# Kernel tuning notes

Hardware: AMD Instinct MI355X
Metric: run time of the kernel (lower is better)

Reference implementation:

```python
import jax, jax.numpy as jnp
import numpy as np

B, P, M, N, H, K, EH = 16, 50, 512, 1024, 64, 20, 200


def setup_inputs() -> dict:
    key = jax.random.key(0)
    ks = jax.random.split(key, 16)
    b = jax.random.normal(ks[0], (B, P, M, 1), jnp.float32)
    A = jax.random.normal(ks[1], (1, P, M, N), jnp.float32) / np.float32(np.sqrt(M))
    # random undirected multigraph on P nodes, stored with both directions
    s = jax.random.randint(ks[2], (B, EH), 0, P)
    off = jax.random.randint(ks[3], (B, EH), 1, P)
    d = (s + off) % P
    edge_index = jnp.stack([jnp.concatenate([s, d], 1), jnp.concatenate([d, s], 1)], 1).astype(jnp.int32)  # [B,2,2*EH]

    def lin(k, fi, fo, scale=None):
        scale = np.float32(1.0 / np.sqrt(fi)) if scale is None else np.float32(scale)
        return jax.random.normal(k, (fi, fo), jnp.float32) * scale, jnp.zeros((fo,), jnp.float32)

    W_e1, b_e1 = lin(ks[4], P * M, P * H)
    W_e2, b_e2 = lin(ks[5], P * H, 2 * P * H)
    W_e3, b_e3 = lin(ks[6], 2 * P * H, 4 * P * H)
    W_c1, b_c1 = lin(ks[7], 4 * H, 2 * H)
    W_c2, b_c2 = lin(ks[8], 2 * H, 2 * H)
    W_f1, b_f1 = lin(ks[9], 2 * H, H)
    W_f2, _ = lin(ks[10], H, K * 4, scale=1e-3)
    b_f2 = jnp.full((K * 4,), -2.0, jnp.float32)  # mimics fc2 init (tiny weights, negative bias)
    max_param = jnp.array([0.01, 0.1, 0.1, 0.1], jnp.float32).reshape(1, 1, 1, 4)  # [alpha,tau,rho,eta]_max
    y0 = jax.random.normal(ks[11], (B, P, N, 1), jnp.float32) * 0.01
    u0 = jax.random.normal(ks[12], (B, P, N, 1), jnp.float32) * 0.01
    d0 = jax.random.normal(ks[13], (B, P, N, 1), jnp.float32) * 0.01
    return dict(b=b, A=A, edge_index=edge_index, max_param=max_param,
                W_e1=W_e1, b_e1=b_e1, W_e2=W_e2, b_e2=b_e2, W_e3=W_e3, b_e3=b_e3,
                W_c1=W_c1, b_c1=b_c1, W_c2=W_c2, b_c2=b_c2,
                W_f1=W_f1, b_f1=b_f1, W_f2=W_f2, b_f2=b_f2,
                y0=y0, u0=u0, d0=d0)


def _lrelu(x):
    return jax.nn.leaky_relu(x, 0.01)


def _gcn(x, s, d, W, bias):
    # GCNConv: sym-normalized propagation with self loops. x: [P,F]
    h = x @ W
    deg = jnp.zeros((x.shape[0],), x.dtype).at[d].add(1.0) + 1.0  # +1 self loop
    dinv = jax.lax.rsqrt(deg)
    agg = jnp.zeros_like(h).at[d].add(h[s] * (dinv[s] * dinv[d])[:, None])
    agg = agg + h * (dinv * dinv)[:, None]  # self-loop term
    return agg + bias


def _delta(y, s, d):
    # nested neighbor loop: for each directed edge (s,d): delta[s]+=y[s]-y[d]; delta[d]-=same
    diff = y[s] - y[d]  # [E,N,1]
    return jnp.zeros_like(y).at[s].add(diff).at[d].add(-diff)


def reference(b, A, edge_index, max_param,
              W_e1, b_e1, W_e2, b_e2, W_e3, b_e3,
              W_c1, b_c1, W_c2, b_c2, W_f1, b_f1, W_f2, b_f2,
              y0, u0, d0):
    Bb = b.shape[0]
    n = A.shape[3]
    k_steps = W_f2.shape[1] // 4
    src, dst = edge_index[:, 0], edge_index[:, 1]

    # ---- GNN hypernetwork ----
    x = b.reshape(Bb, -1)
    x = _lrelu(x @ W_e1 + b_e1)
    x = _lrelu(x @ W_e2 + b_e2)
    x = (x @ W_e3 + b_e3).reshape(Bb, P, -1)  # [B,P,4H]
    x = _lrelu(jax.vmap(lambda xf, s, d: _gcn(xf, s, d, W_c1, b_c1))(x, src, dst))
    x = _lrelu(jax.vmap(lambda xf, s, d: _gcn(xf, s, d, W_c2, b_c2))(x, src, dst))
    x = x.mean(axis=1)  # global_mean_pool over nodes
    x = _lrelu(x @ W_f1 + b_f1)
    hyp = (x @ W_f2 + b_f2).reshape(Bb, k_steps, 1, 4)
    hyp = jax.nn.sigmoid(jnp.cumsum(hyp, axis=1)) * max_param  # [B,K,1,4]
    hyp_scan = jnp.transpose(hyp, (1, 3, 0, 2))[..., None, None]  # [K,4,B,1,1,1]

    # ---- precompute ----
    A0 = A[0]  # [P,M,N]
    AtA = jnp.einsum('pmn,pmk->pnk', A0, A0)  # [P,N,N]
    Atb = jnp.einsum('pmn,bpmo->bpno', A0, b)  # [B,P,N,1]
    sum_nb = jax.vmap(lambda s: jnp.zeros((P,), b.dtype).at[s].add(1.0))(src)[:, :, None, None]  # [B,P,1,1]

    # ---- unrolled D-ADMM / DLASSO ----
    def step(carry, hk):
        y_k, U_k, dlt = carry
        alpha, tau, rho, eta = hk[0], hk[1], hk[2], hk[3]
        AtAy = jnp.einsum('pnk,bpko->bpno', AtA, y_k)
        g = AtAy - Atb + jnp.sign(y_k) * tau + U_k * sum_nb + dlt * rho
        y_n = y_k - alpha * g
        dlt_n = jax.vmap(_delta)(y_n, src, dst)
        U_n = U_k + dlt_n * eta
        return (y_n, U_n, dlt_n), y_n

    _, Y = jax.lax.scan(step, (y0, u0, d0), hyp_scan)
    return Y  # [K,B,P,N,1]
```

## Files before the change

kernel.cpp:

```cpp
#include <hip/hip_runtime.h>

namespace {
constexpr int NB = 16;
constexpr int NP = 50;
constexpr int NM = 512;
constexpr int NN = 1024;
constexpr int NK = 20;
constexpr long ASZ = (long)NP * NM * NN;
constexpr long YSZ = (long)NB * NP * NN;
}

typedef __attribute__((ext_vector_type(8))) short bf16x8;
typedef __attribute__((ext_vector_type(4))) float f32x4;

__device__ __forceinline__ float lrelu(float x){ return x > 0.f ? x : 0.01f*x; }
__device__ __forceinline__ unsigned short f2bf(float f){
  unsigned u = __builtin_bit_cast(unsigned, f);
  u += 0x7fffu + ((u >> 16) & 1u);
  return (unsigned short)(u >> 16);
}

__global__ __launch_bounds__(256) void k_prep(const float* __restrict__ A,
                      unsigned short* __restrict__ abf, unsigned short* __restrict__ abfT){
  const int p = blockIdx.x, mt = blockIdx.y, nt = blockIdx.z;
  const int tid = threadIdx.x;
  __shared__ unsigned short tile[64][72];
  const int m0 = mt*64, n0 = nt*64;
  {
    int r = tid>>2, cs = (tid&3)*16;
    const float* src = A + ((long)p*NM + m0 + r)*NN + n0 + cs;
    unsigned short tmp[16];
    #pragma unroll
    for (int q=0;q<16;q+=4){
      float4 v = *(const float4*)(src+q);
      tmp[q+0]=f2bf(v.x); tmp[q+1]=f2bf(v.y); tmp[q+2]=f2bf(v.z); tmp[q+3]=f2bf(v.w);
    }
    #pragma unroll
    for (int q=0;q<16;q++) tile[r][cs+q] = tmp[q];
    unsigned short* dst = abf + ((long)p*NM + m0 + r)*NN + n0 + cs;
    #pragma unroll
    for (int q=0;q<16;q+=8) *(uint4*)(dst+q) = *(const uint4*)&tmp[q];
  }
  __syncthreads();
  {
    int r = tid>>2, cs = (tid&3)*16;
    unsigned short* dst = abfT + ((long)p*NN + n0 + r)*NM + m0 + cs;
    unsigned short tmp[16];
    #pragma unroll
    for (int q=0;q<16;q++) tmp[q] = tile[cs+q][r];
    #pragma unroll
    for (int q=0;q<16;q+=8) *(uint4*)(dst+q) = *(const uint4*)&tmp[q];
  }
}

__global__ void k_init(const float* __restrict__ y0, const float* __restrict__ u0,
                       const float* __restrict__ d0, float* __restrict__ y,
                       float* __restrict__ u, float* __restrict__ dl,
                       unsigned short* __restrict__ ybf, int n){
  int e = (blockIdx.x*blockDim.x + threadIdx.x)*4;
  if (e >= n) return;
  float4 a = *(const float4*)(y0+e);
  *(float4*)(y+e) = a;
  ushort4 o; o.x=f2bf(a.x); o.y=f2bf(a.y); o.z=f2bf(a.z); o.w=f2bf(a.w);
  *(ushort4*)(ybf+e) = o;
  *(float4*)(u+e)  = *(const float4*)(u0+e);
  *(float4*)(dl+e) = *(const float4*)(d0+e);
}

__global__ __launch_bounds__(256) void k_enc2(const float* __restrict__ X, const float* __restrict__ W,
                           float* __restrict__ part, int fi, int fo, int ichunk, int actin){
  const int tid = threadIdx.x;
  const int o0 = (blockIdx.x*256 + tid)*4;
  const int c  = blockIdx.y;
  const bool ok = o0 < fo;
  __shared__ float xs[64][16];
  float4 acc[16];
  #pragma unroll
  for (int b=0;b<16;b++){ acc[b].x=0.f; acc[b].y=0.f; acc[b].z=0.f; acc[b].w=0.f; }
  const long ibase = (long)c*ichunk;
  const int xb = tid&15, xio = (tid>>4)*4;
  for (int s=0; s<ichunk; s+=64){
    float4 v = *(const float4*)(X + (long)xb*fi + ibase + s + xio);
    if (actin){ v.x=lrelu(v.x); v.y=lrelu(v.y); v.z=lrelu(v.z); v.w=lrelu(v.w); }
    __syncthreads();
    xs[xio+0][xb]=v.x; xs[xio+1][xb]=v.y; xs[xio+2][xb]=v.z; xs[xio+3][xb]=v.w;
    __syncthreads();
    const float* wp = W + (ibase+s)*fo + o0;
    #pragma unroll 4
    for (int i=0;i<64;i++){
      float4 w;
      if (ok) w = *(const float4*)(wp + (long)i*fo);
      else { w.x=0.f; w.y=0.f; w.z=0.f; w.w=0.f; }
      #pragma unroll
      for (int b2=0;b2<16;b2+=4){
        float4 x4 = *(const float4*)&xs[i][b2];
        acc[b2+0].x += w.x*x4.x; acc[b2+0].y += w.y*x4.x; acc[b2+0].z += w.z*x4.x; acc[b2+0].w += w.w*x4.x;
        acc[b2+1].x += w.x*x4.y; acc[b2+1].y += w.y*x4.y; acc[b2+1].z += w.z*x4.y; acc[b2+1].w += w.w*x4.y;
        acc[b2+2].x += w.x*x4.z; acc[b2+2].y += w.y*x4.z; acc[b2+2].z += w.z*x4.z; acc[b2+2].w += w.w*x4.z;
        acc[b2+3].x += w.x*x4.w; acc[b2+3].y += w.y*x4.w; acc[b2+3].z += w.z*x4.w; acc[b2+3].w += w.w*x4.w;
      }
    }
  }
  if (ok){
    float* pp = part + ((long)c*16)*fo + o0;
    #pragma unroll
    for (int b=0;b<16;b++) *(float4*)(pp + (long)b*fo) = acc[b];
  }
}

__global__ void k_enc_reduce(const float* __restrict__ part, const float* __restrict__ bias,
                             float* __restrict__ out, int fo, int nchunk){
  int i = blockIdx.x*256 + threadIdx.x;
  if (i >= 16*fo) return;
  int o = i % fo;
  float s = bias[o];
  for (int c=0;c<nchunk;c++) s += part[(long)c*16*fo + i];
  out[i] = s;
}

__global__ __launch_bounds__(64) void k_graph(const int* __restrict__ ei, float* __restrict__ adjg,
                        float* __restrict__ dmg, float* __restrict__ snbg){
  const int b = blockIdx.x, tid = threadIdx.x;
  __shared__ float adj[2500], dm[2500], deg[50], dinv[50], snb[50];
  for (int i=tid;i<2500;i+=64){ adj[i]=0.f; dm[i]=0.f; }
  if (tid<50){ deg[tid]=0.f; snb[tid]=0.f; }
  __syncthreads();
  const int* e = ei + b*800;
  for (int k=tid;k<400;k+=64){
    atomicAdd(&deg[e[400+k]], 1.f);
    atomicAdd(&snb[e[k]], 1.f);
  }
  __syncthreads();
  if (tid<50) dinv[tid] = 1.f / sqrtf(deg[tid] + 1.f);
  __syncthreads();
  for (int k=tid;k<400;k+=64){
    int s = e[k], d = e[400+k];
    atomicAdd(&adj[d*50+s], dinv[s]*dinv[d]);
    atomicAdd(&dm[s*50+s],  1.f); atomicAdd(&dm[s*50+d], -1.f);
    atomicAdd(&dm[d*50+d],  1.f); atomicAdd(&dm[d*50+s], -1.f);
  }
  __syncthreads();
  if (tid<50) adj[tid*50+tid] += dinv[tid]*dinv[tid];
  __syncthreads();
  for (int i=tid;i<2500;i+=64){ adjg[b*2500+i]=adj[i]; dmg[b*2500+i]=dm[i]; }
  if (tid<50) snbg[b*50+tid]=snb[tid];
}

__global__ __launch_bounds__(256) void k_gnn(const float* __restrict__ h3,
     const float* __restrict__ Wc1, const float* __restrict__ bc1,
     const float* __restrict__ Wc2, const float* __restrict__ bc2,
     const float* __restrict__ Wf1, const float* __restrict__ bf1,
     const float* __restrict__ Wf2, const float* __restrict__ bf2,
     const float* __restrict__ maxp, const float* __restrict__ adjg,
     float* __restrict__ hypg){
  const int b = blockIdx.x, tid = threadIdx.x;
  __shared__ float adj[2500];
  __shared__ float bufA[6400];
  __shared__ float bufB[6400];
  __shared__ float xm[128], hv1[64], raw[80];
  for (int i=tid;i<2500;i+=256) adj[i] = adjg[b*2500+i];

  const int j = tid & 127, nh = tid >> 7;
  float acc[25];
  #pragma unroll
  for (int q=0;q<25;q++) acc[q]=0.f;
  for (int ic=0; ic<4; ic++){
    __syncthreads();
    for (int e=tid; e<800; e+=256){
      int n = e>>4, seg = (e&15)*4;
      *(float4*)&bufB[n*64+seg] = *(const float4*)(h3 + (long)b*12800 + n*256 + ic*64 + seg);
    }
    __syncthreads();
    for (int i=0;i<64;i+=4){
      float w0 = Wc1[(long)(ic*64+i+0)*128 + j];
      float w1 = Wc1[(long)(ic*64+i+1)*128 + j];
      float w2 = Wc1[(long)(ic*64+i+2)*128 + j];
      float w3 = Wc1[(long)(ic*64+i+3)*128 + j];
      #pragma unroll
      for (int q=0;q<25;q++){
        float4 xv = *(const float4*)&bufB[(nh*25+q)*64 + i];
        acc[q] += xv.x*w0 + xv.y*w1 + xv.z*w2 + xv.w*w3;
      }
    }
  }
  __syncthreads();
  #pragma unroll
  for (int q=0;q<25;q++) bufA[(nh*25+q)*128 + j] = acc[q];
  __syncthreads();
  {
    float a2[25];
    float bv = bc1[j];
    #pragma unroll
    for (int q=0;q<25;q++) a2[q]=bv;
    for (int qq=0; qq<50; qq++){
      float hvv = bufA[qq*128 + j];
      #pragma unroll
      for (int q=0;q<25;q++) a2[q] += adj[(nh*25+q)*50 + qq]*hvv;
    }
    __syncthreads();
    #pragma unroll
    for (int q=0;q<25;q++) bufB[(nh*25+q)*128 + j] = lrelu(a2[q]);
  }
  __syncthreads();
  {
    float a2[25];
    #pragma unroll
    for (int q=0;q<25;q++) a2[q]=0.f;
    for (int i=0;i<128;i+=4){
      float w0 = Wc2[(long)(i+0)*128 + j];
      float w1 = Wc2[(long)(i+1)*128 + j];
      float w2 = Wc2[(long)(i+2)*128 + j];
      float w3 = Wc2[(long)(i+3)*128 + j];
      #pragma unroll
      for (int q=0;q<25;q++){
        float4 xv = *(const float4*)&bufB[(nh*25+q)*128 + i];
        a2[q] += xv.x*w0 + xv.y*w1 + xv.z*w2 + xv.w*w3;
      }
    }
    __syncthreads();
    #pragma unroll
    for (int q=0;q<25;q++) bufA[(nh*25+q)*128 + j] = a2[q];
  }
  __syncthreads();
  {
    float a2[25];
    float bv = bc2[j];
    #pragma unroll
    for (int q=0;q<25;q++) a2[q]=bv;
    for (int qq=0; qq<50; qq++){
      float hvv = bufA[qq*128 + j];
      #pragma unroll
      for (int q=0;q<25;q++) a2[q] += adj[(nh*25+q)*50 + qq]*hvv;
    }
    __syncthreads();
    #pragma unroll
    for (int q=0;q<25;q++) bufB[(nh*25+q)*128 + j] = lrelu(a2[q]);
  }
  __syncthreads();
  if (tid < 128){
    float s = 0.f;
    for (int n=0;n<50;n++) s += bufB[n*128 + tid];
    xm[tid] = s * (1.f/50.f);
  }
  __syncthreads();
  if (tid < 64){
    float s = bf1[tid];
    for (int i=0;i<128;i++) s += xm[i]*Wf1[i*64 + tid];
    hv1[tid] = lrelu(s);
  }
  __syncthreads();
  if (tid < 80){
    float s = bf2[tid];
    for (int i=0;i<64;i++) s += hv1[i]*Wf2[i*80 + tid];
    raw[tid] = s;
  }
  __syncthreads();
  if (tid < 4){
    float c = 0.f;
    for (int k=0;k<20;k++){
      c += raw[k*4 + tid];
      hypg[b*80 + k*4 + tid] = maxp[tid] / (1.f + expf(-c));
    }
  }
}

__global__ __launch_bounds__(256) void k_g1m(const unsigned short* __restrict__ abf,
                      const unsigned short* __restrict__ ybf, unsigned short* __restrict__ tbf){
  const int p = blockIdx.x;
  const int tid = threadIdx.x, wave = tid>>6, lane = tid&63;
  __shared__ unsigned short ylds[16][1032];
  {
    int b = tid>>4, c0 = (tid&15)*8;
    const unsigned short* yr = ybf + ((long)b*NP + p)*NN;
    #pragma unroll
    for (int it=0; it<8; it++)
      *(uint4*)&ylds[b][it*128 + c0] = *(const uint4*)(yr + it*128 + c0);
  }
  __syncthreads();
  const int lr = lane&15, kg = lane>>4;
  const int mt0 = blockIdx.y*4 + wave;
  const int m0 = mt0*16, m1 = (mt0+16)*16;
  const unsigned short* a0 = abf + ((long)p*NM + m0 + lr)*NN + kg*8;
  const unsigned short* a1 = abf + ((long)p*NM + m1 + lr)*NN + kg*8;
  const unsigned short* yp = &ylds[lr][kg*8];
  f32x4 acc0a={0.f,0.f,0.f,0.f}, acc0b={0.f,0.f,0.f,0.f};
  f32x4 acc1a={0.f,0.f,0.f,0.f}, acc1b={0.f,0.f,0.f,0.f};
  #pragma unroll 4
  for (int ks=0; ks<32; ks+=2){
    bf16x8 y0 = *(const bf16x8*)(yp + ks*32);
    bf16x8 y1 = *(const bf16x8*)(yp + ks*32 + 32);
    bf16x8 a00 = *(const bf16x8*)(a0 + (long)ks*32);
    bf16x8 a01 = *(const bf16x8*)(a0 + (long)ks*32 + 32);
    bf16x8 a10 = *(const bf16x8*)(a1 + (long)ks*32);
    bf16x8 a11 = *(const bf16x8*)(a1 + (long)ks*32 + 32);
    acc0a = __builtin_amdgcn_mfma_f32_16x16x32_bf16(a00, y0, acc0a, 0, 0, 0);
    acc1a = __builtin_amdgcn_mfma_f32_16x16x32_bf16(a10, y0, acc1a, 0, 0, 0);
    acc0b = __builtin_amdgcn_mfma_f32_16x16x32_bf16(a01, y1, acc0b, 0, 0, 0);
    acc1b = __builtin_amdgcn_mfma_f32_16x16x32_bf16(a11, y1, acc1b, 0, 0, 0);
  }
  f32x4 acc0 = acc0a + acc0b;
  f32x4 acc1 = acc1a + acc1b;
  #pragma unroll
  for (int r=0;r<4;r++){
    tbf[((long)lr*NP + p)*NM + m0 + kg*4 + r] = f2bf(acc0[r]);
    tbf[((long)lr*NP + p)*NM + m1 + kg*4 + r] = f2bf(acc1[r]);
  }
}

template<bool BF16IN>
__global__ __launch_bounds__(256) void k_gatm(const unsigned short* __restrict__ abfT,
                      const void* __restrict__ srcv, float* __restrict__ z){
  const int p = blockIdx.x;
  const int tid = threadIdx.x, wave = tid>>6, lane = tid&63;
  __shared__ unsigned short tlds[16][520];
  {
    int b = tid>>4, c0 = (tid&15)*8;
    if constexpr (BF16IN){
      const unsigned short* tr = (const unsigned short*)srcv + ((long)b*NP + p)*NM;
      #pragma unroll
      for (int it=0; it<4; it++)
        *(uint4*)&tlds[b][it*128 + c0] = *(const uint4*)(tr + it*128 + c0);
    } else {
      const float* tr = (const float*)srcv + ((long)b*NP + p)*NM;
      #pragma unroll
      for (int it=0; it<4; it++){
        float4 lo = *(const float4*)(tr + it*128 + c0);
        float4 hi = *(const float4*)(tr + it*128 + c0 + 4);
        unsigned short w[8];
        w[0]=f2bf(lo.x); w[1]=f2bf(lo.y); w[2]=f2bf(lo.z); w[3]=f2bf(lo.w);
        w[4]=f2bf(hi.x); w[5]=f2bf(hi.y); w[6]=f2bf(hi.z); w[7]=f2bf(hi.w);
        *(uint4*)&tlds[b][it*128 + c0] = *(const uint4*)w;
      }
    }
  }
  __syncthreads();
  const int lr = lane&15, kg = lane>>4;
  const int nt0 = blockIdx.y*4 + wave;
  const int n0 = nt0*16, n1 = (nt0+32)*16;
  const unsigned short* b0 = abfT + ((long)p*NN + n0 + lr)*NM + kg*8;
  const unsigned short* b1 = abfT + ((long)p*NN + n1 + lr)*NM + kg*8;
  const unsigned short* tp = &tlds[lr][kg*8];
  f32x4 acc0a={0.f,0.f,0.f,0.f}, acc0b={0.f,0.f,0.f,0.f};
  f32x4 acc1a={0.f,0.f,0.f,0.f}, acc1b={0.f,0.f,0.f,0.f};
  #pragma unroll 4
  for (int ks=0; ks<16; ks+=2){
    bf16x8 t0 = *(const bf16x8*)(tp + ks*32);
    bf16x8 t1 = *(const bf16x8*)(tp + ks*32 + 32);
    bf16x8 b00 = *(const bf16x8*)(b0 + (long)ks*32);
    bf16x8 b01 = *(const bf16x8*)(b0 + (long)ks*32 + 32);
    bf16x8 b10 = *(const bf16x8*)(b1 + (long)ks*32);
    bf16x8 b11 = *(const bf16x8*)(b1 + (long)ks*32 + 32);
    acc0a = __builtin_amdgcn_mfma_f32_16x16x32_bf16(t0, b00, acc0a, 0, 0, 0);
    acc1a = __builtin_amdgcn_mfma_f32_16x16x32_bf16(t0, b10, acc1a, 0, 0, 0);
    acc0b = __builtin_amdgcn_mfma_f32_16x16x32_bf16(t1, b01, acc0b, 0, 0, 0);
    acc1b = __builtin_amdgcn_mfma_f32_16x16x32_bf16(t1, b11, acc1b, 0, 0, 0);
  }
  f32x4 acc0 = acc0a + acc0b;
  f32x4 acc1 = acc1a + acc1b;
  #pragma unroll
  for (int r=0;r<4;r++){
    int bb = kg*4 + r;
    z[((long)bb*NP + p)*NN + n0 + lr] = acc0[r];
    z[((long)bb*NP + p)*NN + n1 + lr] = acc1[r];
  }
}

__global__ __launch_bounds__(256) void k_upd(const float* __restrict__ zz, const float* __restrict__ atb,
                      const float* __restrict__ dmg, const float* __restrict__ snbg,
                      const float* __restrict__ hypg, int k,
                      float* __restrict__ y, unsigned short* __restrict__ ybf,
                      float* __restrict__ u, float* __restrict__ dl,
                      float* __restrict__ yout){
  const int b = blockIdx.x;
  const int n0 = blockIdx.y*128;
  const int tid = threadIdx.x;
  __shared__ float yn[50][128];
  __shared__ float dms[2500];
  __shared__ float sa[4];
  if (tid<4) sa[tid] = hypg[b*80 + k*4 + tid];
  for (int i=tid;i<2500;i+=256) dms[i] = dmg[b*2500+i];
  __syncthreads();
  const float alpha = sa[0], tau = sa[1], rho = sa[2], eta = sa[3];
  for (int e=tid; e<6400; e+=256){
    const int p = e>>7, nn = e&127;
    const long idx = ((long)b*NP + p)*NN + n0 + nn;
    float yv = y[idx];
    float g = zz[idx] - atb[idx]
            + ((yv>0.f)?1.f:((yv<0.f)?-1.f:0.f))*tau
            + u[idx]*snbg[b*NP+p] + dl[idx]*rho;
    float ynv = yv - alpha*g;
    yn[p][nn] = ynv;
    y[idx] = ynv;
    ybf[idx] = f2bf(ynv);
    yout[(long)k*YSZ + idx] = ynv;
  }
  __syncthreads();
  for (int e=tid; e<6400; e+=256){
    const int p = e>>7, nn = e&127;
    float s = 0.f;
    #pragma unroll 10
    for (int q=0;q<NP;q++) s += dms[p*50+q]*yn[q][nn];
    const long idx = ((long)b*NP + p)*NN + n0 + nn;
    dl[idx] = s;
    u[idx] += s*eta;
  }
}

extern "C" void kernel_launch(void* const* d_in, const int* in_sizes, int n_in,
                              void* d_out, int out_size, void* d_ws, size_t ws_size,
                              hipStream_t stream){
  (void)in_sizes; (void)n_in; (void)out_size; (void)ws_size;
  const float* bin = (const float*)d_in[0];
  const float* A   = (const float*)d_in[1];
  const int*   ei  = (const int*)d_in[2];
  const float* mxp = (const float*)d_in[3];
  const float* We1 = (const float*)d_in[4];  const float* be1 = (const float*)d_in[5];
  const float* We2 = (const float*)d_in[6];  const float* be2 = (const float*)d_in[7];
  const float* We3 = (const float*)d_in[8];  const float* be3 = (const float*)d_in[9];
  const float* Wc1 = (const float*)d_in[10]; const float* bc1 = (const float*)d_in[11];
  const float* Wc2 = (const float*)d_in[12]; const float* bc2 = (const float*)d_in[13];
  const float* Wf1 = (const float*)d_in[14]; const float* bf1 = (const float*)d_in[15];
  const float* Wf2 = (const float*)d_in[16]; const float* bf2 = (const float*)d_in[17];
  const float* y0  = (const float*)d_in[18];
  const float* u0  = (const float*)d_in[19];
  const float* dd0 = (const float*)d_in[20];
  float* out = (float*)d_out;

  char* cur = (char*)d_ws;
  auto alloc = [&](size_t bytes)->void*{
    void* pp = (void*)cur; cur += (bytes + 255) & ~(size_t)255; return pp;
  };
  unsigned short* abf  = (unsigned short*)alloc(ASZ*2);
  unsigned short* abfT = (unsigned short*)alloc(ASZ*2);
  float* atb = (float*)alloc(YSZ*4);
  float* y   = (float*)alloc(YSZ*4);
  unsigned short* ybf = (unsigned short*)alloc(YSZ*2);
  float* u   = (float*)alloc(YSZ*4);
  float* dl  = (float*)alloc(YSZ*4);
  unsigned short* tbf = (unsigned short*)alloc((size_t)NB*NP*NM*2);
  float* z   = (float*)alloc(YSZ*4);
  float* h1  = (float*)alloc((size_t)16*3200*4);
  float* h2  = (float*)alloc((size_t)16*6400*4);
  float* h3  = (float*)alloc((size_t)16*12800*4);
  float* adj = (float*)alloc((size_t)16*2500*4);
  float* dm  = (float*)alloc((size_t)16*2500*4);
  float* snb = (float*)alloc((size_t)16*50*4);
  float* hyp = (float*)alloc((size_t)16*80*4);
  float* part= (float*)alloc((size_t)21000000);

  k_prep<<<dim3(50,8,16), dim3(256), 0, stream>>>(A, abf, abfT);
  k_init<<<dim3(800), dim3(256), 0, stream>>>(y0, u0, dd0, y, u, dl, ybf, (int)YSZ);
  k_gatm<false><<<dim3(50,8), dim3(256), 0, stream>>>(abfT, bin, atb);

  k_enc2<<<dim3(4,50),  dim3(256), 0, stream>>>(bin, We1, part, 25600, 3200, 512, 0);
  k_enc_reduce<<<dim3(200), dim3(256), 0, stream>>>(part, be1, h1, 3200, 50);
  k_enc2<<<dim3(7,25),  dim3(256), 0, stream>>>(h1, We2, part, 3200, 6400, 128, 1);
  k_enc_reduce<<<dim3(400), dim3(256), 0, stream>>>(part, be2, h2, 6400, 25);
  k_enc2<<<dim3(13,25), dim3(256), 0, stream>>>(h2, We3, part, 6400, 12800, 256, 1);
  k_enc_reduce<<<dim3(800), dim3(256), 0, stream>>>(part, be3, h3, 12800, 25);

  k_graph<<<dim3(16), dim3(64), 0, stream>>>(ei, adj, dm, snb);
  k_gnn<<<dim3(16), dim3(256), 0, stream>>>(h3, Wc1, bc1, Wc2, bc2, Wf1, bf1, Wf2, bf2, mxp, adj, hyp);

  for (int k=0;k<NK;k++){
    k_g1m<<<dim3(50,4),  dim3(256), 0, stream>>>(abf, ybf, tbf);
    k_gatm<true><<<dim3(50,8), dim3(256), 0, stream>>>(abfT, tbf, z);
    k_upd<<<dim3(16,8),  dim3(256), 0, stream>>>(z, atb, dm, snb, hyp, k, y, ybf, u, dl, out);
  }
}
```

Before: 1.440 ms.

## Precompute AtA per node and fuse gradient matvec with ADMM update

Instead of applying A and then A^T each iteration (two bf16 GEMV-like passes over the 50x512x1024 A), a one-time MFMA kernel forms the symmetric AtA (50x1024x1024, bf16), writing both triangles. Each iteration then does one AtA*y product fused with the y-update, followed by a separate delta/U kernel, using ping-pong bf16 y buffers. The change removes the per-iteration intermediate and the A^T pass, but reads a larger matrix (2x A bytes) each step and adds an upfront O(P·N²·M) GEMM plus an extra bf16 rounding of AtA.

After: 1.514 ms. 1.05x slower.

```diff
diff --git a/kernel.cpp b/kernel.cpp
--- a/kernel.cpp
+++ b/kernel.cpp
@@ -21,7 +21,7 @@
 }
 
 __global__ __launch_bounds__(256) void k_prep(const float* __restrict__ A,
-                      unsigned short* __restrict__ abf, unsigned short* __restrict__ abfT){
+                      unsigned short* __restrict__ abfT){
   const int p = blockIdx.x, mt = blockIdx.y, nt = blockIdx.z;
   const int tid = threadIdx.x;
   __shared__ unsigned short tile[64][72];
@@ -37,9 +37,6 @@
     }
     #pragma unroll
     for (int q=0;q<16;q++) tile[r][cs+q] = tmp[q];
-    unsigned short* dst = abf + ((long)p*NM + m0 + r)*NN + n0 + cs;
-    #pragma unroll
-    for (int q=0;q<16;q+=8) *(uint4*)(dst+q) = *(const uint4*)&tmp[q];
   }
   __syncthreads();
   {
@@ -67,270 +64,22 @@
   *(float4*)(dl+e) = *(const float4*)(d0+e);
 }
 
-__global__ __launch_bounds__(256) void k_enc2(const float* __restrict__ X, const float* __restrict__ W,
-                           float* __restrict__ part, int fi, int fo, int ichunk, int actin){
-  const int tid = threadIdx.x;
-  const int o0 = (blockIdx.x*256 + tid)*4;
-  const int c  = blockIdx.y;
-  const bool ok = o0 < fo;
-  __shared__ float xs[64][16];
-  float4 acc[16];
-  #pragma unroll
-  for (int b=0;b<16;b++){ acc[b].x=0.f; acc[b].y=0.f; acc[b].z=0.f; acc[b].w=0.f; }
-  const long ibase = (long)c*ichunk;
-  const int xb = tid&15, xio = (tid>>4)*4;
-  for (int s=0; s<ichunk; s+=64){
-    float4 v = *(const float4*)(X + (long)xb*fi + ibase + s + xio);
-    if (actin){ v.x=lrelu(v.x); v.y=lrelu(v.y); v.z=lrelu(v.z); v.w=lrelu(v.w); }
-    __syncthreads();
-    xs[xio+0][xb]=v.x; xs[xio+1][xb]=v.y; xs[xio+2][xb]=v.z; xs[xio+3][xb]=v.w;
-    __syncthreads();
-    const float* wp = W + (ibase+s)*fo + o0;
-    #pragma unroll 4
-    for (int i=0;i<64;i++){
-      float4 w;
-      if (ok) w = *(const float4*)(wp + (long)i*fo);
-      else { w.x=0.f; w.y=0.f; w.z=0.f; w.w=0.f; }
-      #pragma unroll
-      for (int b2=0;b2<16;b2+=4){
-        float4 x4 = *(const float4*)&xs[i][b2];
-        acc[b2+0].x += w.x*x4.x; acc[b2+0].y += w.y*x4.x; acc[b2+0].z += w.z*x4.x; acc[b2+0].w += w.w*x4.x;
-        acc[b2+1].x += w.x*x4.y; acc[b2+1].y += w.y*x4.y; acc[b2+1].z += w.z*x4.y; acc[b2+1].w += w.w*x4.y;
-        acc[b2+2].x += w.x*x4.z; acc[b2+2].y += w.y*x4.z; acc[b2+2].z += w.z*x4.z; acc[b2+2].w += w.w*x4.z;
-        acc[b2+3].x += w.x*x4.w; acc[b2+3].y += w.y*x4.w; acc[b2+3].z += w.z*x4.w; acc[b2+3].w += w.w*x4.w;
-      }
-    }
-  }
-  if (ok){
-    float* pp = part + ((long)c*16)*fo + o0;
-    #pragma unroll
-    for (int b=0;b<16;b++) *(float4*)(pp + (long)b*fo) = acc[b];
-  }
-}
-
-__global__ void k_enc_reduce(const float* __restrict__ part, const float* __restrict__ bias,
-                             float* __restrict__ out, int fo, int nchunk){
-  int i = blockIdx.x*256 + threadIdx.x;
-  if (i >= 16*fo) return;
-  int o = i % fo;
-  float s = bias[o];
-  for (int c=0;c<nchunk;c++) s += part[(long)c*16*fo + i];
-  out[i] = s;
-}
-
-__global__ __launch_bounds__(64) void k_graph(const int* __restrict__ ei, float* __restrict__ adjg,
-                        float* __restrict__ dmg, float* __restrict__ snbg){
-  const int b = blockIdx.x, tid = threadIdx.x;
-  __shared__ float adj[2500], dm[2500], deg[50], dinv[50], snb[50];
-  for (int i=tid;i<2500;i+=64){ adj[i]=0.f; dm[i]=0.f; }
-  if (tid<50){ deg[tid]=0.f; snb[tid]=0.f; }
-  __syncthreads();
-  const int* e = ei + b*800;
-  for (int k=tid;k<400;k+=64){
-    atomicAdd(&deg[e[400+k]], 1.f);
-    atomicAdd(&snb[e[k]], 1.f);
-  }
-  __syncthreads();
-  if (tid<50) dinv[tid] = 1.f / sqrtf(deg[tid] + 1.f);
-  __syncthreads();
-  for (int k=tid;k<400;k+=64){
-    int s = e[k], d = e[400+k];
-    atomicAdd(&adj[d*50+s], dinv[s]*dinv[d]);
-    atomicAdd(&dm[s*50+s],  1.f); atomicAdd(&dm[s*50+d], -1.f);
-    atomicAdd(&dm[d*50+d],  1.f); atomicAdd(&dm[d*50+s], -1.f);
-  }
-  __syncthreads();
-  if (tid<50) adj[tid*50+tid] += dinv[tid]*dinv[tid];
-  __syncthreads();
-  for (int i=tid;i<2500;i+=64){ adjg[b*2500+i]=adj[i]; dmg[b*2500+i]=dm[i]; }
-  if (tid<50) snbg[b*50+tid]=snb[tid];
-}
-
-__global__ __launch_bounds__(256) void k_gnn(const float* __restrict__ h3,
-     const float* __restrict__ Wc1, const float* __restrict__ bc1,
-     const float* __restrict__ Wc2, const float* __restrict__ bc2,
-     const float* __restrict__ Wf1, const float* __restrict__ bf1,
-     const float* __restrict__ Wf2, const float* __restrict__ bf2,
-     const float* __restrict__ maxp, const float* __restrict__ adjg,
-     float* __restrict__ hypg){
-  const int b = blockIdx.x, tid = threadIdx.x;
-  __shared__ float adj[2500];
-  __shared__ float bufA[6400];
-  __shared__ float bufB[6400];
-  __shared__ float xm[128], hv1[64], raw[80];
-  for (int i=tid;i<2500;i+=256) adj[i] = adjg[b*2500+i];
-
-  const int j = tid & 127, nh = tid >> 7;
-  float acc[25];
-  #pragma unroll
-  for (int q=0;q<25;q++) acc[q]=0.f;
-  for (int ic=0; ic<4; ic++){
-    __syncthreads();
-    for (int e=tid; e<800; e+=256){
-      int n = e>>4, seg = (e&15)*4;
-      *(float4*)&bufB[n*64+seg] = *(const float4*)(h3 + (long)b*12800 + n*256 + ic*64 + seg);
-    }
-    __syncthreads();
-    for (int i=0;i<64;i+=4){
-      float w0 = Wc1[(long)(ic*64+i+0)*128 + j];
-      float w1 = Wc1[(long)(ic*64+i+1)*128 + j];
-      float w2 = Wc1[(long)(ic*64+i+2)*128 + j];
-      float w3 = Wc1[(long)(ic*64+i+3)*128 + j];
-      #pragma unroll
-      for (int q=0;q<25;q++){
-        float4 xv = *(const float4*)&bufB[(nh*25+q)*64 + i];
-        acc[q] += xv.x*w0 + xv.y*w1 + xv.z*w2 + xv.w*w3;
-      }
-    }
-  }
-  __syncthreads();
-  #pragma unroll
-  for (int q=0;q<25;q++) bufA[(nh*25+q)*128 + j] = acc[q];
-  __syncthreads();
-  {
-    float a2[25];
-    float bv = bc1[j];
-    #pragma unroll
-    for (int q=0;q<25;q++) a2[q]=bv;
-    for (int qq=0; qq<50; qq++){
-      float hvv = bufA[qq*128 + j];
-      #pragma unroll
-      for (int q=0;q<25;q++) a2[q] += adj[(nh*25+q)*50 + qq]*hvv;
-    }
-    __syncthreads();
-    #pragma unroll
-    for (int q=0;q<25;q++) bufB[(nh*25+q)*128 + j] = lrelu(a2[q]);
-  }
-  __syncthreads();
-  {
-    float a2[25];
-    #pragma unroll
-    for (int q=0;q<25;q++) a2[q]=0.f;
-    for (int i=0;i<128;i+=4){
-      float w0 = Wc2[(long)(i+0)*128 + j];
-      float w1 = Wc2[(long)(i+1)*128 + j];
-      float w2 = Wc2[(long)(i+2)*128 + j];
-      float w3 = Wc2[(long)(i+3)*128 + j];
-      #pragma unroll
-      for (int q=0;q<25;q++){
-        float4 xv = *(const float4*)&bufB[(nh*25+q)*128 + i];
-        a2[q] += xv.x*w0 + xv.y*w1 + xv.z*w2 + xv.w*w3;
-      }
-    }
-    __syncthreads();
-    #pragma unroll
-    for (int q=0;q<25;q++) bufA[(nh*25+q)*128 + j] = a2[q];
-  }
-  __syncthreads();
-  {
-    float a2[25];
-    float bv = bc2[j];
-    #pragma unroll
-    for (int q=0;q<25;q++) a2[q]=bv;
-    for (int qq=0; qq<50; qq++){
-      float hvv = bufA[qq*128 + j];
-      #pragma unroll
-      for (int q=0;q<25;q++) a2[q] += adj[(nh*25+q)*50 + qq]*hvv;
-    }
-    __syncthreads();
-    #pragma unroll
-    for (int q=0;q<25;q++) bufB[(nh*25+q)*128 + j] = lrelu(a2[q]);
-  }
-  __syncthreads();
-  if (tid < 128){
-    float s = 0.f;
-    for (int n=0;n<50;n++) s += bufB[n*128 + tid];
-    xm[tid] = s * (1.f/50.f);
-  }
-  __syncthreads();
-  if (tid < 64){
-    float s = bf1[tid];
-    for (int i=0;i<128;i++) s += xm[i]*Wf1[i*64 + tid];
-    hv1[tid] = lrelu(s);
-  }
-  __syncthreads();
-  if (tid < 80){
-    float s = bf2[tid];
-    for (int i=0;i<64;i++) s += hv1[i]*Wf2[i*80 + tid];
-    raw[tid] = s;
-  }
-  __syncthreads();
-  if (tid < 4){
-    float c = 0.f;
-    for (int k=0;k<20;k++){
-      c += raw[k*4 + tid];
-      hypg[b*80 + k*4 + tid] = maxp[tid] / (1.f + expf(-c));
-    }
-  }
-}
-
-__global__ __launch_bounds__(256) void k_g1m(const unsigned short* __restrict__ abf,
-                      const unsigned short* __restrict__ ybf, unsigned short* __restrict__ tbf){
-  const int p = blockIdx.x;
-  const int tid = threadIdx.x, wave = tid>>6, lane = tid&63;
-  __shared__ unsigned short ylds[16][1032];
-  {
-    int b = tid>>4, c0 = (tid&15)*8;
-    const unsigned short* yr = ybf + ((long)b*NP + p)*NN;
-    #pragma unroll
-    for (int it=0; it<8; it++)
-      *(uint4*)&ylds[b][it*128 + c0] = *(const uint4*)(yr + it*128 + c0);
-  }
-  __syncthreads();
-  const int lr = lane&15, kg = lane>>4;
-  const int mt0 = blockIdx.y*4 + wave;
-  const int m0 = mt0*16, m1 = (mt0+16)*16;
-  const unsigned short* a0 = abf + ((long)p*NM + m0 + lr)*NN + kg*8;
-  const unsigned short* a1 = abf + ((long)p*NM + m1 + lr)*NN + kg*8;
-  const unsigned short* yp = &ylds[lr][kg*8];
-  f32x4 acc0a={0.f,0.f,0.f,0.f}, acc0b={0.f,0.f,0.f,0.f};
-  f32x4 acc1a={0.f,0.f,0.f,0.f}, acc1b={0.f,0.f,0.f,0.f};
-  #pragma unroll 4
-  for (int ks=0; ks<32; ks+=2){
-    bf16x8 y0 = *(const bf16x8*)(yp + ks*32);
-    bf16x8 y1 = *(const bf16x8*)(yp + ks*32 + 32);
-    bf16x8 a00 = *(const bf16x8*)(a0 + (long)ks*32);
-    bf16x8 a01 = *(const bf16x8*)(a0 + (long)ks*32 + 32);
-    bf16x8 a10 = *(const bf16x8*)(a1 + (long)ks*32);
-    bf16x8 a11 = *(const bf16x8*)(a1 + (long)ks*32 + 32);
-    acc0a = __builtin_amdgcn_mfma_f32_16x16x32_bf16(a00, y0, acc0a, 0, 0, 0);
-    acc1a = __builtin_amdgcn_mfma_f32_16x16x32_bf16(a10, y0, acc1a, 0, 0, 0);
-    acc0b = __builtin_amdgcn_mfma_f32_16x16x32_bf16(a01, y1, acc0b, 0, 0, 0);
-    acc1b = __builtin_amdgcn_mfma_f32_16x16x32_bf16(a11, y1, acc1b, 0, 0, 0);
-  }
-  f32x4 acc0 = acc0a + acc0b;
-  f32x4 acc1 = acc1a + acc1b;
-  #pragma unroll
-  for (int r=0;r<4;r++){
-    tbf[((long)lr*NP + p)*NM + m0 + kg*4 + r] = f2bf(acc0[r]);
-    tbf[((long)lr*NP + p)*NM + m1 + kg*4 + r] = f2bf(acc1[r]);
-  }
-}
-
-template<bool BF16IN>
-__global__ __launch_bounds__(256) void k_gatm(const unsigned short* __restrict__ abfT,
-                      const void* __restrict__ srcv, float* __restrict__ z){
+__global__ __launch_bounds__(256) void k_atb(const unsigned short* __restrict__ abfT,
+                      const float* __restrict__ src, float* __restrict__ z){
   const int p = blockIdx.x;
   const int tid = threadIdx.x, wave = tid>>6, lane = tid&63;
   __shared__ unsigned short tlds[16][520];
   {
     int b = tid>>4, c0 = (tid&15)*8;
-    if constexpr (BF16IN){
-      const unsigned short* tr = (const unsigned short*)srcv + ((long)b*NP + p)*NM;
-      #pragma unroll
-      for (int it=0; it<4; it++)
-        *(uint4*)&tlds[b][it*128 + c0] = *(const uint4*)(tr + it*128 + c0);
-    } else {
-      const float* tr = (const float*)srcv + ((long)b*NP + p)*NM;
-      #pragma unroll
-      for (int it=0; it<4; it++){
-        float4 lo = *(const float4*)(tr + it*128 + c0);
-        float4 hi = *(const float4*)(tr + it*128 + c0 + 4);
-        unsigned short w[8];
-        w[0]=f2bf(lo.x); w[1]=f2bf(lo.y); w[2]=f2bf(lo.z); w[3]=f2bf(lo.w);
-        w[4]=f2bf(hi.x); w[5]=f2bf(hi.y); w[6]=f2bf(hi.z); w[7]=f2bf(hi.w);
-        *(uint4*)&tlds[b][it*128 + c0] = *(const uint4*)w;
-      }
+    const float* tr = src + ((long)b*NP + p)*NM;
+    #pragma unroll
+    for (int it=0; it<4; it++){
+      float4 lo = *(const float4*)(tr + it*128 + c0);
+      float4 hi = *(const float4*)(tr + it*128 + c0 + 4);
+      unsigned short w[8];
+      w[0]=f2bf(lo.x); w[1]=f2bf(lo.y); w[2]=f2bf(lo.z); w[3]=f2bf(lo.w);
+      w[4]=f2bf(hi.x); w[5]=f2bf(hi.y); w[6]=f2bf(hi.z); w[7]=f2bf(hi.w);
+      *(uint4*)&tlds[b][it*128 + c0] = *(const uint4*)w;
     }
   }
   __syncthreads();
@@ -365,44 +114,351 @@
   }
 }
 
-__global__ __launch_bounds__(256) void k_upd(const float* __restrict__ zz, const float* __restrict__ atb,
-                      const float* __restrict__ dmg, const float* __restrict__ snbg,
-                      const float* __restrict__ hypg, int k,
-                      float* __restrict__ y, unsigned short* __restrict__ ybf,
-                      float* __restrict__ u, float* __restrict__ dl,
-                      float* __restrict__ yout){
-  const int b = blockIdx.x;
-  const int n0 = blockIdx.y*128;
+__global__ __launch_bounds__(256) void k_ata(const unsigned short* __restrict__ abfT,
+                      unsigned short* __restrict__ ata){
+  const int p = blockIdx.x;
+  int yy = blockIdx.y, bi = 0;
+  while (yy >= 8 - bi){ yy -= 8 - bi; bi++; }
+  const int bj = bi + yy;
+  const int i0 = bi*128, j0 = bj*128;
+  const int tid = threadIdx.x, wave = tid>>6, lane = tid&63;
+  const int lr = lane&15, kg = lane>>4;
+  __shared__ unsigned short pa[128][72];
+  __shared__ unsigned short pb[128][72];
+  f32x4 acc[2][8];
+  #pragma unroll
+  for (int ti=0;ti<2;ti++)
+    #pragma unroll
+    for (int tj=0;tj<8;tj++) acc[ti][tj] = (f32x4){0.f,0.f,0.f,0.f};
+  const unsigned short* Abase = abfT + (long)p*NN*NM;
+  for (int mc=0; mc<NM; mc+=64){
+    __syncthreads();
+    {
+      int r = tid>>1, c0 = (tid&1)*32;
+      const unsigned short* sa = Abase + (long)(i0 + r)*NM + mc + c0;
+      const unsigned short* sb = Abase + (long)(j0 + r)*NM + mc + c0;
+      #pragma unroll
+      for (int q=0;q<32;q+=8){
+        *(uint4*)&pa[r][c0+q] = *(const uint4*)(sa+q);
+        *(uint4*)&pb[r][c0+q] = *(const uint4*)(sb+q);
+      }
+    }
+    __syncthreads();
+    #pragma unroll
+    for (int ks=0; ks<2; ks++){
+      bf16x8 av0 = *(const bf16x8*)&pa[wave*32      + lr][ks*32 + kg*8];
+      bf16x8 av1 = *(const bf16x8*)&pa[wave*32 + 16 + lr][ks*32 + kg*8];
+      #pragma unroll
+      for (int tj=0;tj<8;tj++){
+        bf16x8 bv = *(const bf16x8*)&pb[tj*16 + lr][ks*32 + kg*8];
+        acc[0][tj] = __builtin_amdgcn_mfma_f32_16x16x32_bf16(av0, bv, acc[0][tj], 0,0,0);
+        acc[1][tj] = __builtin_amdgcn_mfma_f32_16x16x32_bf16(av1, bv, acc[1][tj], 0,0,0);
+      }
+    }
+  }
+  const long pbase = (long)p << 20;
+  #pragma unroll
+  for (int ti=0; ti<2; ti++){
+    const int ib = i0 + wave*32 + ti*16;
+    #pragma unroll
+    for (int tj=0; tj<8; tj++){
+      const int jb = j0 + tj*16;
+      unsigned short w[4];
+      #pragma unroll
+      for (int r=0;r<4;r++) w[r] = f2bf(acc[ti][tj][r]);
+      #pragma unroll
+      for (int r=0;r<4;r++)
+        ata[pbase + (long)(ib + kg*4 + r)*1024 + jb + lr] = w[r];
+      if (bi != bj)
+        *(ushort4*)(ata + pbase + (long)(jb + lr)*1024 + ib + kg*4) = *(const ushort4*)w;
+    }
+  }
+}
+
+__global__ __launch_bounds__(256) void k_enc2(const float* __restrict__ X, const float* __restrict__ W,
+                           float* __restrict__ part, int fi, int fo, int ichunk, int actin){
   const int tid = threadIdx.x;
-  __shared__ float yn[50][128];
+  const int o0 = (blockIdx.x*256 + tid)*4;
+  const int c  = blockIdx.y;
+  const bool ok = o0 < fo;
+  __shared__ float xs[64][16];
+  float4 acc[16];
+  #pragma unroll
+  for (int b=0;b<16;b++){ acc[b].x=0.f; acc[b].y=0.f; acc[b].z=0.f; acc[b].w=0.f; }
+  const long ibase = (long)c*ichunk;
+  const int xb = tid&15, xio = (tid>>4)*4;
+  for (int s=0; s<ichunk; s+=64){
+    float4 v = *(const float4*)(X + (long)xb*fi + ibase + s + xio);
+    if (actin){ v.x=lrelu(v.x); v.y=lrelu(v.y); v.z=lrelu(v.z); v.w=lrelu(v.w); }
+    __syncthreads();
+    xs[xio+0][xb]=v.x; xs[xio+1][xb]=v.y; xs[xio+2][xb]=v.z; xs[xio+3][xb]=v.w;
+    __syncthreads();
+    const float* wp = W + (ibase+s)*fo + o0;
+    #pragma unroll 4
+    for (int i=0;i<64;i++){
+      float4 w;
+      if (ok) w = *(const float4*)(wp + (long)i*fo);
+      else { w.x=0.f; w.y=0.f; w.z=0.f; w.w=0.f; }
+      #pragma unroll
+      for (int b2=0;b2<16;b2+=4){
+        float4 x4 = *(const float4*)&xs[i][b2];
+        acc[b2+0].x += w.x*x4.x; acc[b2+0].y += w.y*x4.x; acc[b2+0].z += w.z*x4.x; acc[b2+0].w += w.w*x4.x;
+        acc[b2+1].x += w.x*x4.y; acc[b2+1].y += w.y*x4.y; acc[b2+1].z += w.z*x4.y; acc[b2+1].w += w.w*x4.y;
+        acc[b2+2].x += w.x*x4.z; acc[b2+2].y += w.y*x4.z; acc[b2+2].z += w.z*x4.z; acc[b2+2].w += w.w*x4.z;
+        acc[b2+3].x += w.x*x4.w; acc[b2+3].y += w.y*x4.w; acc[b2+3].z += w.z*x4.w; acc[b2+3].w += w.w*x4.w;
+      }
+    }
+  }
+  if (ok){
+    float* pp = part + ((long)c*16)*fo + o0;
+    #pragma unroll
+    for (int b=0;b<16;b++) *(float4*)(pp + (long)b*fo) = acc[b];
+  }
+}
+
+__global__ void k_enc_reduce(const float* __restrict__ part, const float* __restrict__ bias,
+                             float* __restrict__ out, int fo, int nchunk){
+  int i = blockIdx.x*256 + threadIdx.x;
+  if (i >= 16*fo) return;
+  int o = i % fo;
+  float s = bias[o];
+  for (int c=0;c<nchunk;c++) s += part[(long)c*16*fo + i];
+  out[i] = s;
+}
+
+__global__ __launch_bounds__(64) void k_graph(const int* __restrict__ ei, float* __restrict__ adjg,
+                        float* __restrict__ dmg, float* __restrict__ snbg){
+  const int b = blockIdx.x, tid = threadIdx.x;
+  __shared__ float adj[2500], dm[2500], deg[50], dinv[50], snb[50];
+  for (int i=tid;i<2500;i+=64){ adj[i]=0.f; dm[i]=0.f; }
+  if (tid<50){ deg[tid]=0.f; snb[tid]=0.f; }
+  __syncthreads();
+  const int* e = ei + b*800;
+  for (int k=tid;k<400;k+=64){
+    atomicAdd(&deg[e[400+k]], 1.f);
+    atomicAdd(&snb[e[k]], 1.f);
+  }
+  __syncthreads();
+  if (tid<50) dinv[tid] = 1.f / sqrtf(deg[tid] + 1.f);
+  __syncthreads();
+  for (int k=tid;k<400;k+=64){
+    int s = e[k], d = e[400+k];
+    atomicAdd(&adj[d*50+s], dinv[s]*dinv[d]);
+    atomicAdd(&dm[s*50+s],  1.f); atomicAdd(&dm[s*50+d], -1.f);
+    atomicAdd(&dm[d*50+d],  1.f); atomicAdd(&dm[d*50+s], -1.f);
+  }
+  __syncthreads();
+  if (tid<50) adj[tid*50+tid] += dinv[tid]*dinv[tid];
+  __syncthreads();
+  for (int i=tid;i<2500;i+=64){ adjg[b*2500+i]=adj[i]; dmg[b*2500+i]=dm[i]; }
+  if (tid<50) snbg[b*50+tid]=snb[tid];
+}
+
+__global__ __launch_bounds__(256) void k_gnn(const float* __restrict__ h3,
+     const float* __restrict__ Wc1, const float* __restrict__ bc1,
+     const float* __restrict__ Wc2, const float* __restrict__ bc2,
+     const float* __restrict__ Wf1, const float* __restrict__ bf1,
+     const float* __restrict__ Wf2, const float* __restrict__ bf2,
+     const float* __restrict__ maxp, const float* __restrict__ adjg,
+     float* __restrict__ hypg){
+  const int b = blockIdx.x, tid = threadIdx.x;
+  __shared__ float adj[2500];
+  __shared__ float bufA[6400];
+  __shared__ float bufB[6400];
+  __shared__ float xm[128], hv1[64], raw[80];
+  for (int i=tid;i<2500;i+=256) adj[i] = adjg[b*2500+i];
+
+  const int j = tid & 127, nh = tid >> 7;
+  float acc[25];
+  #pragma unroll
+  for (int q=0;q<25;q++) acc[q]=0.f;
+  for (int ic=0; ic<4; ic++){
+    __syncthreads();
+    for (int e=tid; e<800; e+=256){
+      int n = e>>4, seg = (e&15)*4;
+      *(float4*)&bufB[n*64+seg] = *(const float4*)(h3 + (long)b*12800 + n*256 + ic*64 + seg);
+    }
+    __syncthreads();
+    for (int i=0;i<64;i+=4){
+      float w0 = Wc1[(long)(ic*64+i+0)*128 + j];
+      float w1 = Wc1[(long)(ic*64+i+1)*128 + j];
+      float w2 = Wc1[(long)(ic*64+i+2)*128 + j];
+      float w3 = Wc1[(long)(ic*64+i+3)*128 + j];
+      #pragma unroll
+      for (int q=0;q<25;q++){
+        float4 xv = *(const float4*)&bufB[(nh*25+q)*64 + i];
+        acc[q] += xv.x*w0 + xv.y*w1 + xv.z*w2 + xv.w*w3;
+      }
+    }
+  }
+  __syncthreads();
+  #pragma unroll
+  for (int q=0;q<25;q++) bufA[(nh*25+q)*128 + j] = acc[q];
+  __syncthreads();
+  {
+    float a2[25];
+    float bv = bc1[j];
+    #pragma unroll
+    for (int q=0;q<25;q++) a2[q]=bv;
+    for (int qq=0; qq<50; qq++){
+      float hvv = bufA[qq*128 + j];
+      #pragma unroll
+      for (int q=0;q<25;q++) a2[q] += adj[(nh*25+q)*50 + qq]*hvv;
+    }
+    __syncthreads();
+    #pragma unroll
+    for (int q=0;q<25;q++) bufB[(nh*25+q)*128 + j] = lrelu(a2[q]);
+  }
+  __syncthreads();
+  {
+    float a2[25];
+    #pragma unroll
+    for (int q=0;q<25;q++) a2[q]=0.f;
+    for (int i=0;i<128;i+=4){
+      float w0 = Wc2[(long)(i+0)*128 + j];
+      float w1 = Wc2[(long)(i+1)*128 + j];
+      float w2 = Wc2[(long)(i+2)*128 + j];
+      float w3 = Wc2[(long)(i+3)*128 + j];
+      #pragma unroll
+      for (int q=0;q<25;q++){
+        float4 xv = *(const float4*)&bufB[(nh*25+q)*128 + i];
+        a2[q] += xv.x*w0 + xv.y*w1 + xv.z*w2 + xv.w*w3;
+      }
+    }
+    __syncthreads();
+    #pragma unroll
+    for (int q=0;q<25;q++) bufA[(nh*25+q)*128 + j] = a2[q];
+  }
+  __syncthreads();
+  {
+    float a2[25];
+    float bv = bc2[j];
+    #pragma unroll
+    for (int q=0;q<25;q++) a2[q]=bv;
+    for (int qq=0; qq<50; qq++){
+      float hvv = bufA[qq*128 + j];
+      #pragma unroll
+      for (int q=0;q<25;q++) a2[q] += adj[(nh*25+q)*50 + qq]*hvv;
+    }
+    __syncthreads();
+    #pragma unroll
+    for (int q=0;q<25;q++) bufB[(nh*25+q)*128 + j] = lrelu(a2[q]);
+  }
+  __syncthreads();
+  if (tid < 128){
+    float s = 0.f;
+    for (int n=0;n<50;n++) s += bufB[n*128 + tid];
+    xm[tid] = s * (1.f/50.f);
+  }
+  __syncthreads();
+  if (tid < 64){
+    float s = bf1[tid];
+    for (int i=0;i<128;i++) s += xm[i]*Wf1[i*64 + tid];
+    hv1[tid] = lrelu(s);
+  }
+  __syncthreads();
+  if (tid < 80){
+    float s = bf2[tid];
+    for (int i=0;i<64;i++) s += hv1[i]*Wf2[i*80 + tid];
+    raw[tid] = s;
+  }
+  __syncthreads();
+  if (tid < 4){
+    float c = 0.f;
+    for (int k=0;k<20;k++){
+      c += raw[k*4 + tid];
+      hypg[b*80 + k*4 + tid] = maxp[tid] / (1.f + expf(-c));
+    }
+  }
+}
+
+__global__ __launch_bounds__(256) void k_z(const unsigned short* __restrict__ ata,
+      const unsigned short* __restrict__ ybin, const float* __restrict__ atb,
+      const float* __restrict__ u, const float* __restrict__ dl,
+      const float* __restrict__ snbg, const float* __restrict__ hypg, int k,
+      float* __restrict__ y, unsigned short* __restrict__ ybout,
+      float* __restrict__ yout){
+  const int p = blockIdx.x;
+  const int tid = threadIdx.x, wave = tid>>6, lane = tid&63;
+  __shared__ unsigned short ylds[16][1032];
+  {
+    int b = tid>>4, c0 = (tid&15)*8;
+    const unsigned short* yr = ybin + ((long)b*NP + p)*NN;
+    #pragma unroll
+    for (int it=0; it<8; it++)
+      *(uint4*)&ylds[b][it*128 + c0] = *(const uint4*)(yr + it*128 + c0);
+  }
+  __syncthreads();
+  const int lr = lane&15, kg = lane>>4;
+  const int nt0 = blockIdx.y*4 + wave;
+  const int n0 = nt0*16, n1 = n0 + 512;
+  const long pb2 = (long)p << 20;
+  const unsigned short* b0 = ata + pb2 + (long)(n0 + lr)*1024 + kg*8;
+  const unsigned short* b1 = ata + pb2 + (long)(n1 + lr)*1024 + kg*8;
+  const unsigned short* yp = &ylds[lr][kg*8];
+  f32x4 acc0a={0.f,0.f,0.f,0.f}, acc0b={0.f,0.f,0.f,0.f};
+  f32x4 acc1a={0.f,0.f,0.f,0.f}, acc1b={0.f,0.f,0.f,0.f};
+  #pragma unroll 4
+  for (int ks=0; ks<32; ks+=2){
+    bf16x8 y0v = *(const bf16x8*)(yp + ks*32);
+    bf16x8 y1v = *(const bf16x8*)(yp + ks*32 + 32);
+    bf16x8 b00 = *(const bf16x8*)(b0 + ks*32);
+    bf16x8 b01 = *(const bf16x8*)(b0 + ks*32 + 32);
+    bf16x8 b10 = *(const bf16x8*)(b1 + ks*32);
+    bf16x8 b11 = *(const bf16x8*)(b1 + ks*32 + 32);
+    acc0a = __builtin_amdgcn_mfma_f32_16x16x32_bf16(y0v, b00, acc0a, 0,0,0);
+    acc1a = __builtin_amdgcn_mfma_f32_16x16x32_bf16(y0v, b10, acc1a, 0,0,0);
+    acc0b = __builtin_amdgcn_mfma_f32_16x16x32_bf16(y1v, b01, acc0b, 0,0,0);
+    acc1b = __builtin_amdgcn_mfma_f32_16x16x32_bf16(y1v, b11, acc1b, 0,0,0);
+  }
+  f32x4 z0 = acc0a + acc0b;
+  f32x4 z1 = acc1a + acc1b;
+  #pragma unroll
+  for (int r=0;r<4;r++){
+    const int b = kg*4 + r;
+    const float4 hp = *(const float4*)(hypg + b*80 + k*4);
+    const float sp = snbg[b*NP + p];
+    const long base = ((long)b*NP + p)*NN;
+    {
+      const long idx = base + n0 + lr;
+      float yv = y[idx];
+      float g = z0[r] - atb[idx] + ((yv>0.f)?1.f:((yv<0.f)?-1.f:0.f))*hp.y
+              + u[idx]*sp + dl[idx]*hp.z;
+      float ynv = yv - hp.x*g;
+      y[idx] = ynv; ybout[idx] = f2bf(ynv); yout[(long)k*YSZ + idx] = ynv;
+    }
+    {
+      const long idx = base + n1 + lr;
+      float yv = y[idx];
+      float g = z1[r] - atb[idx] + ((yv>0.f)?1.f:((yv<0.f)?-1.f:0.f))*hp.y
+              + u[idx]*sp + dl[idx]*hp.z;
+      float ynv = yv - hp.x*g;
+      y[idx] = ynv; ybout[idx] = f2bf(ynv); yout[(long)k*YSZ + idx] = ynv;
+    }
+  }
+}
+
+__global__ __launch_bounds__(256) void k_dm(const float* __restrict__ dmg,
+      const float* __restrict__ hypg, int k, const float* __restrict__ y,
+      float* __restrict__ u, float* __restrict__ dl){
+  const int b = blockIdx.x, n0 = blockIdx.y*128, tid = threadIdx.x;
+  __shared__ float ys[50][128];
   __shared__ float dms[2500];
-  __shared__ float sa[4];
-  if (tid<4) sa[tid] = hypg[b*80 + k*4 + tid];
   for (int i=tid;i<2500;i+=256) dms[i] = dmg[b*2500+i];
-  __syncthreads();
-  const float alpha = sa[0], tau = sa[1], rho = sa[2], eta = sa[3];
   for (int e=tid; e<6400; e+=256){
-    const int p = e>>7, nn = e&127;
-    const long idx = ((long)b*NP + p)*NN + n0 + nn;
-    float yv = y[idx];
-    float g = zz[idx] - atb[idx]
-            + ((yv>0.f)?1.f:((yv<0.f)?-1.f:0.f))*tau
-            + u[idx]*snbg[b*NP+p] + dl[idx]*rho;
-    float ynv = yv - alpha*g;
-    yn[p][nn] = ynv;
-    y[idx] = ynv;
-    ybf[idx] = f2bf(ynv);
-    yout[(long)k*YSZ + idx] = ynv;
-  }
-  __syncthreads();
+    int p=e>>7, nn=e&127;
+    ys[p][nn] = y[((long)b*NP+p)*NN + n0 + nn];
+  }
+  __syncthreads();
+  const float eta = hypg[b*80 + k*4 + 3];
   for (int e=tid; e<6400; e+=256){
-    const int p = e>>7, nn = e&127;
-    float s = 0.f;
+    int p=e>>7, nn=e&127;
+    float s=0.f;
     #pragma unroll 10
-    for (int q=0;q<NP;q++) s += dms[p*50+q]*yn[q][nn];
-    const long idx = ((long)b*NP + p)*NN + n0 + nn;
-    dl[idx] = s;
-    u[idx] += s*eta;
+    for (int q=0;q<NP;q++) s += dms[p*50+q]*ys[q][nn];
+    long idx = ((long)b*NP+p)*NN + n0 + nn;
+    dl[idx]=s;
+    u[idx]+=s*eta;
   }
 }
 
@@ -430,15 +486,14 @@
   auto alloc = [&](size_t bytes)->void*{
     void* pp = (void*)cur; cur += (bytes + 255) & ~(size_t)255; return pp;
   };
-  unsigned short* abf  = (unsigned short*)alloc(ASZ*2);
   unsigned short* abfT = (unsigned short*)alloc(ASZ*2);
+  unsigned short* ata  = (unsigned short*)alloc((size_t)NP*1024*1024*2);
   float* atb = (float*)alloc(YSZ*4);
   float* y   = (float*)alloc(YSZ*4);
-  unsigned short* ybf = (unsigned short*)alloc(YSZ*2);
+  unsigned short* ybf0 = (unsigned short*)alloc(YSZ*2);
+  unsigned short* ybf1 = (unsigned short*)alloc(YSZ*2);
   float* u   = (float*)alloc(YSZ*4);
   float* dl  = (float*)alloc(YSZ*4);
-  unsigned short* tbf = (unsigned short*)alloc((size_t)NB*NP*NM*2);
-  float* z   = (float*)alloc(YSZ*4);
   float* h1  = (float*)alloc((size_t)16*3200*4);
   float* h2  = (float*)alloc((size_t)16*6400*4);
   float* h3  = (float*)alloc((size_t)16*12800*4);
@@ -448,9 +503,10 @@
   float* hyp = (float*)alloc((size_t)16*80*4);
   float* part= (float*)alloc((size_t)21000000);
 
-  k_prep<<<dim3(50,8,16), dim3(256), 0, stream>>>(A, abf, abfT);
-  k_init<<<dim3(800), dim3(256), 0, stream>>>(y0, u0, dd0, y, u, dl, ybf, (int)YSZ);
-  k_gatm<false><<<dim3(50,8), dim3(256), 0, stream>>>(abfT, bin, atb);
+  k_prep<<<dim3(50,8,16), dim3(256), 0, stream>>>(A, abfT);
+  k_init<<<dim3(800), dim3(256), 0, stream>>>(y0, u0, dd0, y, u, dl, ybf0, (int)YSZ);
+  k_atb<<<dim3(50,8), dim3(256), 0, stream>>>(abfT, bin, atb);
+  k_ata<<<dim3(50,36), dim3(256), 0, stream>>>(abfT, ata);
 
   k_enc2<<<dim3(4,50),  dim3(256), 0, stream>>>(bin, We1, part, 25600, 3200, 512, 0);
   k_enc_reduce<<<dim3(200), dim3(256), 0, stream>>>(part, be1, h1, 3200, 50);
@@ -463,8 +519,9 @@
   k_gnn<<<dim3(16), dim3(256), 0, stream>>>(h3, Wc1, bc1, Wc2, bc2, Wf1, bf1, Wf2, bf2, mxp, adj, hyp);
 
   for (int k=0;k<NK;k++){
-    k_g1m<<<dim3(50,4),  dim3(256), 0, stream>>>(abf, ybf, tbf);
-    k_gatm<true><<<dim3(50,8), dim3(256), 0, stream>>>(abfT, tbf, z);
-    k_upd<<<dim3(16,8),  dim3(256), 0, stream>>>(z, atb, dm, snb, hyp, k, y, ybf, u, dl, out);
-  }
-}
+    const unsigned short* ybin = (k & 1) ? ybf1 : ybf0;
+    unsigned short* ybout      = (k & 1) ? ybf0 : ybf1;
+    k_z <<<dim3(50,8), dim3(256), 0, stream>>>(ata, ybin, atb, u, dl, snb, hyp, k, y, ybout, out);
+    k_dm<<<dim3(16,8), dim3(256), 0, stream>>>(dm, hyp, k, y, u, dl);
+  }
+}
```
